# Kernel tuning notes

Hardware: AMD Instinct MI355X
Metric: run time of the kernel (lower is better)

The kernel has to match this reference:

```python
import jax, jax.numpy as jnp
import numpy as np

N_IN, N_H0, N_H1, N_H2, N_H3, N_OUT = 512, 1024, 1024, 1024, 512, 128
B, T = 128, 512
STD = 0.05


def setup_inputs() -> dict:
    key = jax.random.key(0)
    ks = jax.random.split(key, 7)
    # torch nn.Linear(in, out, bias=False) stores weight as [out, in]
    return {
        "input_spikes": jax.random.uniform(ks[0], (B, T, N_IN), dtype=jnp.float32),
        "W_in_h0": STD * jax.random.normal(ks[1], (N_H0, N_IN), dtype=jnp.float32),
        "W_h0_h1": STD * jax.random.normal(ks[2], (N_H1, N_H0), dtype=jnp.float32),
        "W_h1_h2": STD * jax.random.normal(ks[3], (N_H2, N_H1), dtype=jnp.float32),
        "W_h2_h2": STD * jax.random.normal(ks[4], (N_H2, N_H2), dtype=jnp.float32),
        "W_h2_h3": STD * jax.random.normal(ks[5], (N_H3, N_H2), dtype=jnp.float32),
        "W_h3_out": STD * jax.random.normal(ks[6], (N_OUT, N_H3), dtype=jnp.float32),
    }


def _lif(current, v, alpha, v_th):
    v = alpha * v + current
    s = (v >= v_th).astype(v.dtype)
    return s, v * (1.0 - s)


def reference(input_spikes, W_in_h0, W_h0_h1, W_h1_h2, W_h2_h2, W_h2_h3, W_h3_out):
    b = input_spikes.shape[0]
    dt = input_spikes.dtype
    z = lambda n: jnp.zeros((b, n), dtype=dt)
    # carry: membrane potentials for h0..h3, out, plus recurrent h2 spikes
    init = (z(N_H0), z(N_H1), z(N_H2), z(N_H3), z(N_OUT), z(N_H2))
    xs = jnp.swapaxes(input_spikes, 0, 1)  # [T, B, N_IN]

    def step(carry, x_t):
        v0, v1, v2, v3, vo, s2_prev = carry
        s0, v0 = _lif(x_t @ W_in_h0.T, v0, 0.9, 0.5)
        s1, v1 = _lif(s0 @ W_h0_h1.T, v1, 0.95, 0.5)
        s2, v2 = _lif(s1 @ W_h1_h2.T + s2_prev @ W_h2_h2.T, v2, 0.93, 0.5)
        s3, v3 = _lif(s2 @ W_h2_h3.T, v3, 0.9, 0.5)
        so, vo = _lif(s3 @ W_h3_out.T, vo, 0.82, 0.8)
        return (v0, v1, v2, v3, vo, s2), so

    _, out = jax.lax.scan(step, init, xs)
    output_spikes = jnp.swapaxes(out, 0, 1)  # [B, T, N_OUT]
    spike_counts = output_spikes.sum(axis=1)  # [B, N_OUT]
    return output_spikes, spike_counts
```

## Files before the change

kernel.cpp:

```cpp
#include <hip/hip_runtime.h>
#include <cstddef>


#define NB 128
#define NT 512

enum : size_t {
  OFF_V0   = 0,
  OFF_V1   = OFF_V0 + 131072,
  OFF_V2   = OFF_V1 + 131072,
  OFF_V3   = OFF_V2 + 131072,
  OFF_VO   = OFF_V3 + 65536,
  OFF_CNT  = OFF_VO + 16384,
  OFF_C2A  = OFF_CNT + 16384,
  OFF_BYTE = OFF_C2A + 262144,
  WS_FLOATS = OFF_BYTE + 229376
};
#define BS0 0
#define BS1 262144
#define BS2 524288
#define BS3 786432

__global__ __launch_bounds__(256) void init_kernel(float* __restrict__ wf) {
  size_t i = (size_t)blockIdx.x * blockDim.x + threadIdx.x;
  size_t stride = (size_t)gridDim.x * blockDim.x;
  for (size_t j = i; j < WS_FLOATS; j += stride) wf[j] = 0.0f;
}

template<bool ABYTE>
__device__ __forceinline__ void gemm_core(
    const void* __restrict__ Abase, int Astride,
    const float* __restrict__ W, int K, int fold,
    int bBase, int oBase,
    float (&As)[2][32][34], float (&Ws)[2][32][34],
    float acc[2][2])
{
  const int tid = threadIdx.x;
  const int ldRow = tid >> 3;
  const int ldK   = (tid & 7) << 2;
  const int tb = (tid & 15) << 1;
  const int to = (tid >> 4) << 1;

  const float* Wrow = W + (size_t)(oBase + ldRow) * K + ldK;
  const unsigned char* Abrow = nullptr;
  const float* Afrow = nullptr;
  if (ABYTE) Abrow = (const unsigned char*)Abase + (size_t)(bBase + ldRow) * Astride + ldK;
  else       Afrow = (const float*)Abase + (size_t)(bBase + ldRow) * Astride + ldK;

  const int NKT = K >> 5;

  float pa[4]; float4 pw;
  {
    float c0, c1, c2, c3;
    if (ABYTE) {
      unsigned int u = *(const unsigned int*)(Abrow);
      c0 = (float)(u & 0xff); c1 = (float)((u >> 8) & 0xff);
      c2 = (float)((u >> 16) & 0xff); c3 = (float)(u >> 24);
    } else {
      float4 f = *(const float4*)(Afrow);
      c0 = f.x; c1 = f.y; c2 = f.z; c3 = f.w;
    }
    float4 cw = *(const float4*)(Wrow);
    As[0][ldK + 0][ldRow] = c0; As[0][ldK + 1][ldRow] = c1;
    As[0][ldK + 2][ldRow] = c2; As[0][ldK + 3][ldRow] = c3;
    Ws[0][ldK + 0][ldRow] = cw.x; Ws[0][ldK + 1][ldRow] = cw.y;
    Ws[0][ldK + 2][ldRow] = cw.z; Ws[0][ldK + 3][ldRow] = cw.w;
  }
  if (NKT > 1) {
    if (ABYTE) {
      unsigned int u = *(const unsigned int*)(Abrow + 32);
      pa[0] = (float)(u & 0xff); pa[1] = (float)((u >> 8) & 0xff);
      pa[2] = (float)((u >> 16) & 0xff); pa[3] = (float)(u >> 24);
    } else {
      float4 f = *(const float4*)(Afrow + 32);
      pa[0] = f.x; pa[1] = f.y; pa[2] = f.z; pa[3] = f.w;
    }
    pw = *(const float4*)(Wrow + 32);
  }
  __syncthreads();

  float tot[2][2] = {{0.f, 0.f}, {0.f, 0.f}};
  float pan[2][2] = {{0.f, 0.f}, {0.f, 0.f}};
  int cb = 0;
  for (int kt = 0; kt < NKT; ++kt) {
    float na[4]; float4 nw;
    if (kt + 2 < NKT) {
      const int ko = (kt + 2) << 5;
      if (ABYTE) {
        unsigned int u = *(const unsigned int*)(Abrow + ko);
        na[0] = (float)(u & 0xff); na[1] = (float)((u >> 8) & 0xff);
        na[2] = (float)((u >> 16) & 0xff); na[3] = (float)(u >> 24);
      } else {
        float4 f = *(const float4*)(Afrow + ko);
        na[0] = f.x; na[1] = f.y; na[2] = f.z; na[3] = f.w;
      }
      nw = *(const float4*)(Wrow + ko);
    }
    if (fold && kt == 16) {
#pragma unroll
      for (int i = 0; i < 2; ++i)
#pragma unroll
        for (int j = 0; j < 2; ++j) {
          tot[i][j] = __fadd_rn(tot[i][j], pan[i][j]);
          pan[i][j] = 0.f;
        }
    }
#pragma unroll
    for (int k = 0; k < 32; ++k) {
      const float2 a = *(const float2*)&As[cb][k][tb];
      const float2 w = *(const float2*)&Ws[cb][k][to];
      pan[0][0] = fmaf(a.x, w.x, pan[0][0]);
      pan[0][1] = fmaf(a.x, w.y, pan[0][1]);
      pan[1][0] = fmaf(a.y, w.x, pan[1][0]);
      pan[1][1] = fmaf(a.y, w.y, pan[1][1]);
    }
    if (kt + 1 < NKT) {
      const int nb = cb ^ 1;
      As[nb][ldK + 0][ldRow] = pa[0]; As[nb][ldK + 1][ldRow] = pa[1];
      As[nb][ldK + 2][ldRow] = pa[2]; As[nb][ldK + 3][ldRow] = pa[3];
      Ws[nb][ldK + 0][ldRow] = pw.x; Ws[nb][ldK + 1][ldRow] = pw.y;
      Ws[nb][ldK + 2][ldRow] = pw.z; Ws[nb][ldK + 3][ldRow] = pw.w;
    }
    if (kt + 2 < NKT) { pa[0] = na[0]; pa[1] = na[1]; pa[2] = na[2]; pa[3] = na[3]; pw = nw; }
    __syncthreads();
    cb ^= 1;
  }
#pragma unroll
  for (int i = 0; i < 2; ++i)
#pragma unroll
    for (int j = 0; j < 2; ++j)
      acc[i][j] = __fadd_rn(tot[i][j], pan[i][j]);
}

__global__ __launch_bounds__(256) void phase_kernel(
    const float* __restrict__ x,
    const float* __restrict__ W0, const float* __restrict__ W1,
    const float* __restrict__ W2a, const float* __restrict__ W2b,
    const float* __restrict__ W3, const float* __restrict__ W4,
    float* __restrict__ wf, float* __restrict__ out, int p)
{
  float* cnt = wf + OFF_CNT;
  float* c2a = wf + OFF_C2A;
  unsigned char* sb = (unsigned char*)(wf + OFF_BYTE);
  const int cur = p & 1, prev = cur ^ 1;

  const int blk = blockIdx.x;
  int g, lb, t, K, N, fold;
  if (blk < 128)      { g = 0; lb = blk;       t = p;     K = 512;  N = 1024; fold = 0; }
  else if (blk < 256) { g = 1; lb = blk - 128; t = p - 1; K = 1024; N = 1024; fold = 1; }
  else if (blk < 384) { g = 2; lb = blk - 256; t = p - 2; K = 1024; N = 1024; fold = 1; }
  else if (blk < 512) { g = 3; lb = blk - 384; t = p - 3; K = 1024; N = 1024; fold = 1; }
  else if (blk < 576) { g = 4; lb = blk - 512; t = p - 4; K = 1024; N = 512;  fold = 1; }
  else                { g = 5; lb = blk - 576; t = p - 5; K = 512;  N = 128;  fold = 0; }
  if (t < 0 || t >= NT) return;

  const int ntO = N >> 5;
  const int bBase = (lb / ntO) << 5;
  const int oBase = (lb % ntO) << 5;

  const float* Wm; const void* Ab; int Astride;
  switch (g) {
    case 0: Wm = W0;  Ab = x + (size_t)t * 512;              Astride = NT * 512; break;
    case 1: Wm = W1;  Ab = sb + BS1 - BS1 + (size_t)prev * 131072; Astride = 1024; break;
    case 2: Wm = W2a; Ab = sb + BS1 + (size_t)prev * 131072; Astride = 1024; break;
    case 3: Wm = W2b; Ab = sb + BS2 + (size_t)prev * 131072; Astride = 1024; break;
    case 4: Wm = W3;  Ab = sb + BS2 + (size_t)prev * 131072; Astride = 1024; break;
    default: Wm = W4; Ab = sb + BS3 + (size_t)prev * 65536;  Astride = 512;  break;
  }

  __shared__ float As[2][32][34];
  __shared__ float Ws[2][32][34];
  float acc[2][2];
  if (g == 0) gemm_core<false>(Ab, Astride, Wm, K, fold, bBase, oBase, As, Ws, acc);
  else        gemm_core<true >(Ab, Astride, Wm, K, fold, bBase, oBase, As, Ws, acc);

  const int tid = threadIdx.x;
  const int tb = (tid & 15) << 1;
  const int to = (tid >> 4) << 1;

  if (g == 2) {
    float* dst = c2a + (size_t)cur * 131072;
#pragma unroll
    for (int i = 0; i < 2; ++i) {
      const int b = bBase + tb + i;
      float2 st; st.x = acc[i][0]; st.y = acc[i][1];
      *(float2*)(dst + (size_t)b * 1024 + oBase + to) = st;
    }
    return;
  }

  float alpha, vth = 0.5f;
  float* v; unsigned char* sOut = nullptr;
  switch (g) {
    case 0: alpha = 0.90f; v = wf + OFF_V0; sOut = sb + BS0 + (size_t)cur * 131072; break;
    case 1: alpha = 0.95f; v = wf + OFF_V1; sOut = sb + BS1 + (size_t)cur * 131072; break;
    case 3: alpha = 0.93f; v = wf + OFF_V2; sOut = sb + BS2 + (size_t)cur * 131072; break;
    case 4: alpha = 0.90f; v = wf + OFF_V3; sOut = sb + BS3 + (size_t)cur * 65536;  break;
    default: alpha = 0.82f; vth = 0.8f; v = wf + OFF_VO; break;
  }
  const float* c2aPrev = c2a + (size_t)prev * 131072;

#pragma unroll
  for (int i = 0; i < 2; ++i) {
    const int b = bBase + tb + i;
    int si[2];
#pragma unroll
    for (int j = 0; j < 2; ++j) {
      const int o = oBase + to + j;
      float cin = acc[i][j];
      if (g == 3)
        cin = __fadd_rn(c2aPrev[(size_t)b * 1024 + o], acc[i][j]);
      float* vp = v + (size_t)b * N + o;
      float vv = __fadd_rn(__fmul_rn(alpha, *vp), cin);
      int s = (vv >= vth) ? 1 : 0;
      float sf = (float)s;
      *vp = __fmul_rn(vv, __fsub_rn(1.0f, sf));
      si[j] = s;
      if (g == 5) {
        out[(size_t)b * (NT * 128) + (size_t)t * 128 + o] = sf;
        cnt[b * 128 + o] = __fadd_rn(cnt[b * 128 + o], sf);
      }
    }
    if (g != 5) {
      *(unsigned short*)(sOut + (size_t)b * N + oBase + to) =
          (unsigned short)(si[0] | (si[1] << 8));
    }
  }
}

__global__ __launch_bounds__(256) void fin_kernel(const float* __restrict__ counts,
                                                  float* __restrict__ out) {
  int i = blockIdx.x * blockDim.x + threadIdx.x;
  if (i < 128 * 128) out[(size_t)128 * NT * 128 + i] = counts[i];
}

extern "C" void kernel_launch(void* const* d_in, const int* in_sizes, int n_in,
                              void* d_out, int out_size, void* d_ws, size_t ws_size,
                              hipStream_t stream) {
  const float* x   = (const float*)d_in[0];
  const float* W0  = (const float*)d_in[1];
  const float* W1  = (const float*)d_in[2];
  const float* W2a = (const float*)d_in[3];
  const float* W2b = (const float*)d_in[4];
  const float* W3  = (const float*)d_in[5];
  const float* W4  = (const float*)d_in[6];
  float* wf  = (float*)d_ws;
  float* out = (float*)d_out;

  init_kernel<<<512, 256, 0, stream>>>(wf);
  for (int p = 0; p < NT + 5; ++p) {
    phase_kernel<<<592, 256, 0, stream>>>(x, W0, W1, W2a, W2b, W3, W4, wf, out, p);
  }
  fin_kernel<<<64, 256, 0, stream>>>(wf + OFF_CNT, out);
}
```

Before: 24.21 ms.

## Use 32x64 output tiles with split-K across two thread groups per block

Output tiles grow from 32x32 to 32x64 per block, which halves the grid from 592 to 296 blocks. For K=1024 layers, each block's two 128-thread halves each compute half of K with 4x4 register tiles and fold partial sums through shared memory. K=512 layers use 4x2 tiles over the whole K. The aim is more reuse per load and fewer blocks per launch, in exchange for lower occupancy, fewer waves on a 256-CU device, and more shared memory.

```diff
diff --git a/kernel.cpp b/kernel.cpp
--- a/kernel.cpp
+++ b/kernel.cpp
@@ -27,109 +27,208 @@
   for (size_t j = i; j < WS_FLOATS; j += stride) wf[j] = 0.0f;
 }
 
-template<bool ABYTE>
-__device__ __forceinline__ void gemm_core(
-    const void* __restrict__ Abase, int Astride,
-    const float* __restrict__ W, int K, int fold,
+__device__ __forceinline__ void wrA8(float (&A)[32][32], int ac, int ar, uint2 u) {
+  A[ac + 0][ar] = (float)(u.x & 0xff);
+  A[ac + 1][ar] = (float)((u.x >> 8) & 0xff);
+  A[ac + 2][ar] = (float)((u.x >> 16) & 0xff);
+  A[ac + 3][ar] = (float)(u.x >> 24);
+  A[ac + 4][ar] = (float)(u.y & 0xff);
+  A[ac + 5][ar] = (float)((u.y >> 8) & 0xff);
+  A[ac + 6][ar] = (float)((u.y >> 16) & 0xff);
+  A[ac + 7][ar] = (float)(u.y >> 24);
+}
+__device__ __forceinline__ void wrW16(float (&Wt)[32][68], int wk, int wr,
+    const float4& w0, const float4& w1, const float4& w2, const float4& w3) {
+  Wt[wk + 0][wr]      = w0.x; Wt[wk + 1][wr]      = w0.y;
+  Wt[wk + 2][wr]      = w0.z; Wt[wk + 3][wr]      = w0.w;
+  Wt[wk + 0][wr + 16] = w1.x; Wt[wk + 1][wr + 16] = w1.y;
+  Wt[wk + 2][wr + 16] = w1.z; Wt[wk + 3][wr + 16] = w1.w;
+  Wt[wk + 0][wr + 32] = w2.x; Wt[wk + 1][wr + 32] = w2.y;
+  Wt[wk + 2][wr + 32] = w2.z; Wt[wk + 3][wr + 32] = w2.w;
+  Wt[wk + 0][wr + 48] = w3.x; Wt[wk + 1][wr + 48] = w3.y;
+  Wt[wk + 2][wr + 48] = w3.z; Wt[wk + 3][wr + 48] = w3.w;
+}
+__device__ __forceinline__ void wrA4f(float (&A)[32][32], int ac4, int ar, float4 f) {
+  A[ac4 + 0][ar] = f.x; A[ac4 + 1][ar] = f.y;
+  A[ac4 + 2][ar] = f.z; A[ac4 + 3][ar] = f.w;
+}
+__device__ __forceinline__ void wrA4b(float (&A)[32][32], int ac4, int ar, unsigned u) {
+  A[ac4 + 0][ar] = (float)(u & 0xff);
+  A[ac4 + 1][ar] = (float)((u >> 8) & 0xff);
+  A[ac4 + 2][ar] = (float)((u >> 16) & 0xff);
+  A[ac4 + 3][ar] = (float)(u >> 24);
+}
+__device__ __forceinline__ void wrW8(float (&Wt)[32][68], int wk2, int wr,
+    const float4& w0, const float4& w1) {
+  Wt[wk2 + 0][wr] = w0.x; Wt[wk2 + 1][wr] = w0.y;
+  Wt[wk2 + 2][wr] = w0.z; Wt[wk2 + 3][wr] = w0.w;
+  Wt[wk2 + 4][wr] = w1.x; Wt[wk2 + 5][wr] = w1.y;
+  Wt[wk2 + 6][wr] = w1.z; Wt[wk2 + 7][wr] = w1.w;
+}
+
+__device__ __forceinline__ void gemm_split(
+    const unsigned char* __restrict__ Abase, int Astride,
+    const float* __restrict__ W,
     int bBase, int oBase,
-    float (&As)[2][32][34], float (&Ws)[2][32][34],
-    float acc[2][2])
+    float (&As)[2][2][32][32], float (&Ws)[2][2][32][68],
+    float (&pan)[4][4])
 {
   const int tid = threadIdx.x;
-  const int ldRow = tid >> 3;
-  const int ldK   = (tid & 7) << 2;
-  const int tb = (tid & 15) << 1;
-  const int to = (tid >> 4) << 1;
-
-  const float* Wrow = W + (size_t)(oBase + ldRow) * K + ldK;
-  const unsigned char* Abrow = nullptr;
-  const float* Afrow = nullptr;
-  if (ABYTE) Abrow = (const unsigned char*)Abase + (size_t)(bBase + ldRow) * Astride + ldK;
-  else       Afrow = (const float*)Abase + (size_t)(bBase + ldRow) * Astride + ldK;
-
-  const int NKT = K >> 5;
-
-  float pa[4]; float4 pw;
+  const int grp = tid >> 7, lt = tid & 127;
+  const int ar = lt >> 2, ac = (lt & 3) << 3;
+  const int wr = lt >> 3, wk = (lt & 7) << 2;
+  const int tb4 = (lt >> 4) << 2;
+  const int to4 = (lt & 15) << 2;
+  const int kb = grp << 9;
+
+  const unsigned char* Arow = Abase + (size_t)(bBase + ar) * Astride + kb + ac;
+  const float* Wr = W + (size_t)(oBase + wr) * 1024 + kb + wk;
+
   {
-    float c0, c1, c2, c3;
-    if (ABYTE) {
-      unsigned int u = *(const unsigned int*)(Abrow);
-      c0 = (float)(u & 0xff); c1 = (float)((u >> 8) & 0xff);
-      c2 = (float)((u >> 16) & 0xff); c3 = (float)(u >> 24);
-    } else {
-      float4 f = *(const float4*)(Afrow);
-      c0 = f.x; c1 = f.y; c2 = f.z; c3 = f.w;
-    }
-    float4 cw = *(const float4*)(Wrow);
-    As[0][ldK + 0][ldRow] = c0; As[0][ldK + 1][ldRow] = c1;
-    As[0][ldK + 2][ldRow] = c2; As[0][ldK + 3][ldRow] = c3;
-    Ws[0][ldK + 0][ldRow] = cw.x; Ws[0][ldK + 1][ldRow] = cw.y;
-    Ws[0][ldK + 2][ldRow] = cw.z; Ws[0][ldK + 3][ldRow] = cw.w;
-  }
-  if (NKT > 1) {
-    if (ABYTE) {
-      unsigned int u = *(const unsigned int*)(Abrow + 32);
-      pa[0] = (float)(u & 0xff); pa[1] = (float)((u >> 8) & 0xff);
-      pa[2] = (float)((u >> 16) & 0xff); pa[3] = (float)(u >> 24);
-    } else {
-      float4 f = *(const float4*)(Afrow + 32);
-      pa[0] = f.x; pa[1] = f.y; pa[2] = f.z; pa[3] = f.w;
-    }
-    pw = *(const float4*)(Wrow + 32);
-  }
+    uint2 a = *(const uint2*)(Arow);
+    float4 w0 = *(const float4*)(Wr);
+    float4 w1 = *(const float4*)(Wr + 16 * 1024);
+    float4 w2 = *(const float4*)(Wr + 32 * 1024);
+    float4 w3 = *(const float4*)(Wr + 48 * 1024);
+    wrA8(As[grp][0], ac, ar, a);
+    wrW16(Ws[grp][0], wk, wr, w0, w1, w2, w3);
+  }
+  uint2 pa = *(const uint2*)(Arow + 32);
+  float4 pw0 = *(const float4*)(Wr + 32);
+  float4 pw1 = *(const float4*)(Wr + 32 + 16 * 1024);
+  float4 pw2 = *(const float4*)(Wr + 32 + 32 * 1024);
+  float4 pw3 = *(const float4*)(Wr + 32 + 48 * 1024);
   __syncthreads();
 
-  float tot[2][2] = {{0.f, 0.f}, {0.f, 0.f}};
-  float pan[2][2] = {{0.f, 0.f}, {0.f, 0.f}};
   int cb = 0;
-  for (int kt = 0; kt < NKT; ++kt) {
-    float na[4]; float4 nw;
-    if (kt + 2 < NKT) {
+#pragma unroll 1
+  for (int kt = 0; kt < 16; ++kt) {
+    uint2 na; float4 nw0, nw1, nw2, nw3;
+    if (kt + 2 < 16) {
       const int ko = (kt + 2) << 5;
-      if (ABYTE) {
-        unsigned int u = *(const unsigned int*)(Abrow + ko);
-        na[0] = (float)(u & 0xff); na[1] = (float)((u >> 8) & 0xff);
-        na[2] = (float)((u >> 16) & 0xff); na[3] = (float)(u >> 24);
-      } else {
-        float4 f = *(const float4*)(Afrow + ko);
-        na[0] = f.x; na[1] = f.y; na[2] = f.z; na[3] = f.w;
-      }
-      nw = *(const float4*)(Wrow + ko);
-    }
-    if (fold && kt == 16) {
-#pragma unroll
-      for (int i = 0; i < 2; ++i)
-#pragma unroll
-        for (int j = 0; j < 2; ++j) {
-          tot[i][j] = __fadd_rn(tot[i][j], pan[i][j]);
-          pan[i][j] = 0.f;
-        }
+      na  = *(const uint2*)(Arow + ko);
+      nw0 = *(const float4*)(Wr + ko);
+      nw1 = *(const float4*)(Wr + ko + 16 * 1024);
+      nw2 = *(const float4*)(Wr + ko + 32 * 1024);
+      nw3 = *(const float4*)(Wr + ko + 48 * 1024);
     }
 #pragma unroll
     for (int k = 0; k < 32; ++k) {
-      const float2 a = *(const float2*)&As[cb][k][tb];
-      const float2 w = *(const float2*)&Ws[cb][k][to];
+      const float4 a = *(const float4*)&As[grp][cb][k][tb4];
+      const float4 w = *(const float4*)&Ws[grp][cb][k][to4];
+      pan[0][0] = fmaf(a.x, w.x, pan[0][0]);
+      pan[0][1] = fmaf(a.x, w.y, pan[0][1]);
+      pan[0][2] = fmaf(a.x, w.z, pan[0][2]);
+      pan[0][3] = fmaf(a.x, w.w, pan[0][3]);
+      pan[1][0] = fmaf(a.y, w.x, pan[1][0]);
+      pan[1][1] = fmaf(a.y, w.y, pan[1][1]);
+      pan[1][2] = fmaf(a.y, w.z, pan[1][2]);
+      pan[1][3] = fmaf(a.y, w.w, pan[1][3]);
+      pan[2][0] = fmaf(a.z, w.x, pan[2][0]);
+      pan[2][1] = fmaf(a.z, w.y, pan[2][1]);
+      pan[2][2] = fmaf(a.z, w.z, pan[2][2]);
+      pan[2][3] = fmaf(a.z, w.w, pan[2][3]);
+      pan[3][0] = fmaf(a.w, w.x, pan[3][0]);
+      pan[3][1] = fmaf(a.w, w.y, pan[3][1]);
+      pan[3][2] = fmaf(a.w, w.z, pan[3][2]);
+      pan[3][3] = fmaf(a.w, w.w, pan[3][3]);
+    }
+    if (kt + 1 < 16) {
+      const int nb = cb ^ 1;
+      wrA8(As[grp][nb], ac, ar, pa);
+      wrW16(Ws[grp][nb], wk, wr, pw0, pw1, pw2, pw3);
+    }
+    if (kt + 2 < 16) { pa = na; pw0 = nw0; pw1 = nw1; pw2 = nw2; pw3 = nw3; }
+    __syncthreads();
+    cb ^= 1;
+  }
+
+  float* foldp = &As[1][0][0][0];
+  if (grp == 1) {
+#pragma unroll
+    for (int i = 0; i < 4; ++i) {
+      float4 st; st.x = pan[i][0]; st.y = pan[i][1];
+      st.z = pan[i][2]; st.w = pan[i][3];
+      *(float4*)&foldp[(i * 128 + lt) * 4] = st;
+    }
+  }
+  __syncthreads();
+  if (grp == 0) {
+#pragma unroll
+    for (int i = 0; i < 4; ++i) {
+      float4 h = *(const float4*)&foldp[(i * 128 + lt) * 4];
+      pan[i][0] = __fadd_rn(pan[i][0], h.x);
+      pan[i][1] = __fadd_rn(pan[i][1], h.y);
+      pan[i][2] = __fadd_rn(pan[i][2], h.z);
+      pan[i][3] = __fadd_rn(pan[i][3], h.w);
+    }
+  }
+}
+
+template<bool AFLOAT>
+__device__ __forceinline__ void gemm_whole(
+    const void* __restrict__ Abase, int Astride,
+    const float* __restrict__ W,
+    int bBase, int oBase,
+    float (&As)[2][2][32][32], float (&Ws)[2][2][32][68],
+    float (&pan)[4][2])
+{
+  const int tid = threadIdx.x;
+  const int ar = tid >> 3, ac4 = (tid & 7) << 2;
+  const int wr = tid >> 2, wk2 = (tid & 3) << 3;
+  const int tb4 = (tid >> 5) << 2;
+  const int to2 = (tid & 31) << 1;
+
+  const float* Af = (const float*)Abase + (size_t)(bBase + ar) * Astride + ac4;
+  const unsigned char* Ab = (const unsigned char*)Abase + (size_t)(bBase + ar) * Astride + ac4;
+  const float* Wr = W + (size_t)(oBase + wr) * 512 + wk2;
+
+  {
+    float4 w0 = *(const float4*)(Wr);
+    float4 w1 = *(const float4*)(Wr + 4);
+    if (AFLOAT) wrA4f(As[0][0], ac4, ar, *(const float4*)(Af));
+    else        wrA4b(As[0][0], ac4, ar, *(const unsigned*)(Ab));
+    wrW8(Ws[0][0], wk2, wr, w0, w1);
+  }
+  float4 paf; unsigned pab;
+  if (AFLOAT) paf = *(const float4*)(Af + 32); else pab = *(const unsigned*)(Ab + 32);
+  float4 pw0 = *(const float4*)(Wr + 32);
+  float4 pw1 = *(const float4*)(Wr + 36);
+  __syncthreads();
+
+  int cb = 0;
+#pragma unroll 1
+  for (int kt = 0; kt < 16; ++kt) {
+    float4 naf; unsigned nab; float4 nw0, nw1;
+    if (kt + 2 < 16) {
+      const int ko = (kt + 2) << 5;
+      if (AFLOAT) naf = *(const float4*)(Af + ko); else nab = *(const unsigned*)(Ab + ko);
+      nw0 = *(const float4*)(Wr + ko);
+      nw1 = *(const float4*)(Wr + ko + 4);
+    }
+#pragma unroll
+    for (int k = 0; k < 32; ++k) {
+      const float4 a = *(const float4*)&As[0][cb][k][tb4];
+      const float2 w = *(const float2*)&Ws[0][cb][k][to2];
       pan[0][0] = fmaf(a.x, w.x, pan[0][0]);
       pan[0][1] = fmaf(a.x, w.y, pan[0][1]);
       pan[1][0] = fmaf(a.y, w.x, pan[1][0]);
       pan[1][1] = fmaf(a.y, w.y, pan[1][1]);
-    }
-    if (kt + 1 < NKT) {
+      pan[2][0] = fmaf(a.z, w.x, pan[2][0]);
+      pan[2][1] = fmaf(a.z, w.y, pan[2][1]);
+      pan[3][0] = fmaf(a.w, w.x, pan[3][0]);
+      pan[3][1] = fmaf(a.w, w.y, pan[3][1]);
+    }
+    if (kt + 1 < 16) {
       const int nb = cb ^ 1;
-      As[nb][ldK + 0][ldRow] = pa[0]; As[nb][ldK + 1][ldRow] = pa[1];
-      As[nb][ldK + 2][ldRow] = pa[2]; As[nb][ldK + 3][ldRow] = pa[3];
-      Ws[nb][ldK + 0][ldRow] = pw.x; Ws[nb][ldK + 1][ldRow] = pw.y;
-      Ws[nb][ldK + 2][ldRow] = pw.z; Ws[nb][ldK + 3][ldRow] = pw.w;
-    }
-    if (kt + 2 < NKT) { pa[0] = na[0]; pa[1] = na[1]; pa[2] = na[2]; pa[3] = na[3]; pw = nw; }
+      if (AFLOAT) wrA4f(As[0][nb], ac4, ar, paf);
+      else        wrA4b(As[0][nb], ac4, ar, pab);
+      wrW8(Ws[0][nb], wk2, wr, pw0, pw1);
+    }
+    if (kt + 2 < 16) { paf = naf; pab = nab; pw0 = nw0; pw1 = nw1; }
     __syncthreads();
     cb ^= 1;
   }
-#pragma unroll
-  for (int i = 0; i < 2; ++i)
-#pragma unroll
-    for (int j = 0; j < 2; ++j)
-      acc[i][j] = __fadd_rn(tot[i][j], pan[i][j]);
 }
 
 __global__ __launch_bounds__(256) void phase_kernel(
@@ -139,92 +238,137 @@
     const float* __restrict__ W3, const float* __restrict__ W4,
     float* __restrict__ wf, float* __restrict__ out, int p)
 {
+  __shared__ float As[2][2][32][32];
+  __shared__ float Ws[2][2][32][68];
+
   float* cnt = wf + OFF_CNT;
   float* c2a = wf + OFF_C2A;
   unsigned char* sb = (unsigned char*)(wf + OFF_BYTE);
   const int cur = p & 1, prev = cur ^ 1;
 
   const int blk = blockIdx.x;
-  int g, lb, t, K, N, fold;
-  if (blk < 128)      { g = 0; lb = blk;       t = p;     K = 512;  N = 1024; fold = 0; }
-  else if (blk < 256) { g = 1; lb = blk - 128; t = p - 1; K = 1024; N = 1024; fold = 1; }
-  else if (blk < 384) { g = 2; lb = blk - 256; t = p - 2; K = 1024; N = 1024; fold = 1; }
-  else if (blk < 512) { g = 3; lb = blk - 384; t = p - 3; K = 1024; N = 1024; fold = 1; }
-  else if (blk < 576) { g = 4; lb = blk - 512; t = p - 4; K = 1024; N = 512;  fold = 1; }
-  else                { g = 5; lb = blk - 576; t = p - 5; K = 512;  N = 128;  fold = 0; }
+  int g, lb, t;
+  if (blk < 64)       { g = 0; lb = blk;       t = p;     }
+  else if (blk < 128) { g = 1; lb = blk - 64;  t = p - 1; }
+  else if (blk < 192) { g = 2; lb = blk - 128; t = p - 2; }
+  else if (blk < 256) { g = 3; lb = blk - 192; t = p - 3; }
+  else if (blk < 288) { g = 4; lb = blk - 256; t = p - 4; }
+  else                { g = 5; lb = blk - 288; t = p - 5; }
   if (t < 0 || t >= NT) return;
 
-  const int ntO = N >> 5;
+  const int ntO = (g == 4) ? 8 : (g == 5) ? 2 : 16;
+  const int N   = (g == 4) ? 512 : (g == 5) ? 128 : 1024;
   const int bBase = (lb / ntO) << 5;
-  const int oBase = (lb % ntO) << 5;
-
-  const float* Wm; const void* Ab; int Astride;
+  const int oBase = (lb % ntO) << 6;
+  const int tid = threadIdx.x;
+
+  if (g == 0 || g == 5) {
+    float pan[4][2] = {{0.f,0.f},{0.f,0.f},{0.f,0.f},{0.f,0.f}};
+    float alpha, vth; float* v;
+    if (g == 0) {
+      gemm_whole<true >(x + (size_t)t * 512, NT * 512, W0, bBase, oBase, As, Ws, pan);
+      alpha = 0.90f; vth = 0.5f; v = wf + OFF_V0;
+    } else {
+      gemm_whole<false>(sb + BS3 + (size_t)prev * 65536, 512, W4, bBase, oBase, As, Ws, pan);
+      alpha = 0.82f; vth = 0.8f; v = wf + OFF_VO;
+    }
+    const int tb4 = (tid >> 5) << 2;
+    const int to2 = (tid & 31) << 1;
+    unsigned char* sOut = sb + BS0 + (size_t)cur * 131072;
+#pragma unroll
+    for (int i = 0; i < 4; ++i) {
+      const int b = bBase + tb4 + i;
+      int si[2];
+#pragma unroll
+      for (int j = 0; j < 2; ++j) {
+        const int o = oBase + to2 + j;
+        float* vp = v + (size_t)b * N + o;
+        float vv = __fadd_rn(__fmul_rn(alpha, *vp), pan[i][j]);
+        int s = (vv >= vth) ? 1 : 0;
+        float sf = (float)s;
+        *vp = __fmul_rn(vv, __fsub_rn(1.0f, sf));
+        si[j] = s;
+        if (g == 5) {
+          out[(size_t)b * (NT * 128) + (size_t)t * 128 + o] = sf;
+          cnt[b * 128 + o] = __fadd_rn(cnt[b * 128 + o], sf);
+        }
+      }
+      if (g == 0) {
+        *(unsigned short*)(sOut + (size_t)b * 1024 + oBase + to2) =
+            (unsigned short)(si[0] | (si[1] << 8));
+      }
+    }
+    return;
+  }
+
+  const unsigned char* Ab; const float* Wm;
   switch (g) {
-    case 0: Wm = W0;  Ab = x + (size_t)t * 512;              Astride = NT * 512; break;
-    case 1: Wm = W1;  Ab = sb + BS1 - BS1 + (size_t)prev * 131072; Astride = 1024; break;
-    case 2: Wm = W2a; Ab = sb + BS1 + (size_t)prev * 131072; Astride = 1024; break;
-    case 3: Wm = W2b; Ab = sb + BS2 + (size_t)prev * 131072; Astride = 1024; break;
-    case 4: Wm = W3;  Ab = sb + BS2 + (size_t)prev * 131072; Astride = 1024; break;
-    default: Wm = W4; Ab = sb + BS3 + (size_t)prev * 65536;  Astride = 512;  break;
-  }
-
-  __shared__ float As[2][32][34];
-  __shared__ float Ws[2][32][34];
-  float acc[2][2];
-  if (g == 0) gemm_core<false>(Ab, Astride, Wm, K, fold, bBase, oBase, As, Ws, acc);
-  else        gemm_core<true >(Ab, Astride, Wm, K, fold, bBase, oBase, As, Ws, acc);
-
-  const int tid = threadIdx.x;
-  const int tb = (tid & 15) << 1;
-  const int to = (tid >> 4) << 1;
+    case 1: Ab = sb + BS0 + (size_t)prev * 131072; Wm = W1;  break;
+    case 2: Ab = sb + BS1 + (size_t)prev * 131072; Wm = W2a; break;
+    case 3: Ab = sb + BS2 + (size_t)prev * 131072; Wm = W2b; break;
+    default: Ab = sb + BS2 + (size_t)prev * 131072; Wm = W3; break;
+  }
+  const int Astride = 1024;
+
+  float pan[4][4];
+#pragma unroll
+  for (int i = 0; i < 4; ++i)
+#pragma unroll
+    for (int j = 0; j < 4; ++j) pan[i][j] = 0.f;
+
+  gemm_split(Ab, Astride, Wm, bBase, oBase, As, Ws, pan);
+
+  if (tid >= 128) return;
+  const int lt = tid;
+  const int tb4 = (lt >> 4) << 2;
+  const int to4 = (lt & 15) << 2;
 
   if (g == 2) {
     float* dst = c2a + (size_t)cur * 131072;
 #pragma unroll
-    for (int i = 0; i < 2; ++i) {
-      const int b = bBase + tb + i;
-      float2 st; st.x = acc[i][0]; st.y = acc[i][1];
-      *(float2*)(dst + (size_t)b * 1024 + oBase + to) = st;
+    for (int i = 0; i < 4; ++i) {
+      const int b = bBase + tb4 + i;
+      float4 st; st.x = pan[i][0]; st.y = pan[i][1];
+      st.z = pan[i][2]; st.w = pan[i][3];
+      *(float4*)(dst + (size_t)b * 1024 + oBase + to4) = st;
     }
     return;
   }
 
-  float alpha, vth = 0.5f;
-  float* v; unsigned char* sOut = nullptr;
+  float alpha; float* v; unsigned char* sOut;
   switch (g) {
-    case 0: alpha = 0.90f; v = wf + OFF_V0; sOut = sb + BS0 + (size_t)cur * 131072; break;
     case 1: alpha = 0.95f; v = wf + OFF_V1; sOut = sb + BS1 + (size_t)cur * 131072; break;
     case 3: alpha = 0.93f; v = wf + OFF_V2; sOut = sb + BS2 + (size_t)cur * 131072; break;
-    case 4: alpha = 0.90f; v = wf + OFF_V3; sOut = sb + BS3 + (size_t)cur * 65536;  break;
-    default: alpha = 0.82f; vth = 0.8f; v = wf + OFF_VO; break;
+    default: alpha = 0.90f; v = wf + OFF_V3; sOut = sb + BS3 + (size_t)cur * 65536; break;
   }
   const float* c2aPrev = c2a + (size_t)prev * 131072;
 
 #pragma unroll
-  for (int i = 0; i < 2; ++i) {
-    const int b = bBase + tb + i;
-    int si[2];
-#pragma unroll
-    for (int j = 0; j < 2; ++j) {
-      const int o = oBase + to + j;
-      float cin = acc[i][j];
-      if (g == 3)
-        cin = __fadd_rn(c2aPrev[(size_t)b * 1024 + o], acc[i][j]);
+  for (int i = 0; i < 4; ++i) {
+    const int b = bBase + tb4 + i;
+    float cin[4];
+    if (g == 3) {
+      float4 ca = *(const float4*)(c2aPrev + (size_t)b * 1024 + oBase + to4);
+      cin[0] = __fadd_rn(ca.x, pan[i][0]);
+      cin[1] = __fadd_rn(ca.y, pan[i][1]);
+      cin[2] = __fadd_rn(ca.z, pan[i][2]);
+      cin[3] = __fadd_rn(ca.w, pan[i][3]);
+    } else {
+      cin[0] = pan[i][0]; cin[1] = pan[i][1];
+      cin[2] = pan[i][2]; cin[3] = pan[i][3];
+    }
+    unsigned packed = 0;
+#pragma unroll
+    for (int j = 0; j < 4; ++j) {
+      const int o = oBase + to4 + j;
       float* vp = v + (size_t)b * N + o;
-      float vv = __fadd_rn(__fmul_rn(alpha, *vp), cin);
-      int s = (vv >= vth) ? 1 : 0;
+      float vv = __fadd_rn(__fmul_rn(alpha, *vp), cin[j]);
+      int s = (vv >= 0.5f) ? 1 : 0;
       float sf = (float)s;
       *vp = __fmul_rn(vv, __fsub_rn(1.0f, sf));
-      si[j] = s;
-      if (g == 5) {
-        out[(size_t)b * (NT * 128) + (size_t)t * 128 + o] = sf;
-        cnt[b * 128 + o] = __fadd_rn(cnt[b * 128 + o], sf);
-      }
-    }
-    if (g != 5) {
-      *(unsigned short*)(sOut + (size_t)b * N + oBase + to) =
-          (unsigned short)(si[0] | (si[1] << 8));
-    }
+      packed |= (unsigned)s << (8 * j);
+    }
+    *(unsigned*)(sOut + (size_t)b * N + oBase + to4) = packed;
   }
 }
 
@@ -249,7 +393,7 @@
 
   init_kernel<<<512, 256, 0, stream>>>(wf);
   for (int p = 0; p < NT + 5; ++p) {
-    phase_kernel<<<592, 256, 0, stream>>>(x, W0, W1, W2a, W2b, W3, W4, wf, out, p);
+    phase_kernel<<<296, 256, 0, stream>>>(x, W0, W1, W2a, W2b, W3, W4, wf, out, p);
   }
   fin_kernel<<<64, 256, 0, stream>>>(wf + OFF_CNT, out);
 }
```

Result: no change. 24.41 ms (+0.9%).
